# Performance work log

Measured on AMD Instinct MI355X. Metric: run time of the kernel, lower is better.

Reference implementation:

```python
import jax, jax.numpy as jnp
import numpy as np

N_NODES = 100000
N_EDGES = 1600000
N_GRAPHS = 1000
NODES_PER_GRAPH = 100
D_IN = 128
D_HID = 128
N_TASKS = 12


def setup_inputs() -> dict:
    key = jax.random.key(0)
    ks = jax.random.split(key, 6)
    X = jax.random.normal(ks[0], (N_NODES, D_IN), dtype=jnp.float32)
    edge_index = jax.random.randint(ks[1], (2, N_EDGES), 0, N_NODES, dtype=jnp.int64)
    graph_sizes = jnp.full((N_GRAPHS,), NODES_PER_GRAPH, dtype=jnp.int64)  # sums to N_NODES
    s0 = (2.0 / D_IN) ** 0.5
    W0 = jax.random.normal(ks[2], (D_IN, D_HID), dtype=jnp.float32) * s0
    b0 = jnp.zeros((D_HID,), dtype=jnp.float32)
    W1 = jax.random.normal(ks[3], (D_HID, D_HID), dtype=jnp.float32) * s0
    b1 = jnp.zeros((D_HID,), dtype=jnp.float32)
    Wf = jax.random.normal(ks[4], (D_HID, N_TASKS), dtype=jnp.float32) * s0
    bf = jnp.zeros((N_TASKS,), dtype=jnp.float32)
    return {"X": X, "edge_index": edge_index, "graph_sizes": graph_sizes,
            "W0": W0, "b0": b0, "W1": W1, "b1": b1, "Wf": Wf, "bf": bf}


def reference(X, edge_index, graph_sizes, W0, b0, W1, b1, Wf, bf):
    src, dst = edge_index[0], edge_index[1]
    n = X.shape[0]

    def gconv(x, W, b):
        # GCN-style message passing with self term: sum_{j->i} (x_j W) + x_i W + b
        xw = x @ W                                                    # [N, d]
        agg = jax.ops.segment_sum(xw[src], dst, num_segments=n)       # [N, d]
        return agg + xw + b

    # stacked conv -> relu -> dropout(eval=identity)
    h = jax.nn.relu(gconv(X, W0, b0))
    h = jax.nn.relu(gconv(h, W1, b1))
    out = jax.nn.sigmoid(h @ Wf + bf)                                  # [N, T]

    # ragged per-graph mean readout as a single segment-mean
    g = graph_sizes.shape[0]
    seg_ids = jnp.repeat(jnp.arange(g), graph_sizes, total_repeat_length=n)
    sums = jax.ops.segment_sum(out, seg_ids, num_segments=g)           # [G, T]
    return sums / graph_sizes[:, None].astype(out.dtype)
```

## Files before the change

### kernel.cpp

```cpp
#include <hip/hip_runtime.h>
#include <math.h>

#define D 128
#define NBUCK_MAX 1024
#define NB_EDGE   128

typedef unsigned short u16;
typedef unsigned int   u32;
typedef __attribute__((ext_vector_type(8))) short short8;
typedef __attribute__((ext_vector_type(4))) float f32x4;

static __device__ __forceinline__ u16 f32_to_bf16(float f) {
    u32 u = __builtin_bit_cast(u32, f);
    u32 r = (u + 0x7FFFu + ((u >> 16) & 1u)) >> 16;
    return (u16)r;
}
static __device__ __forceinline__ u32 pack_bf16x2(float lo, float hi) {
    return (u32)f32_to_bf16(lo) | ((u32)f32_to_bf16(hi) << 16);
}
static __device__ __forceinline__ float bf16lo_to_f32(u32 v) {
    return __builtin_bit_cast(float, v << 16);
}
static __device__ __forceinline__ float bf16hi_to_f32(u32 v) {
    return __builtin_bit_cast(float, v & 0xFFFF0000u);
}


__global__ __launch_bounds__(512) void bucket_count(const int* __restrict__ dst, int E, int nbuck,
                                                    int* __restrict__ blockHist) {
    __shared__ int h[NBUCK_MAX];
    int tid = threadIdx.x;
    for (int i = tid; i < nbuck; i += 512) h[i] = 0;
    __syncthreads();
    int per = (E + NB_EDGE - 1) / NB_EDGE;
    int s = blockIdx.x * per, e = min(E, s + per);
    for (int i = s + tid; i < e; i += 512) atomicAdd(&h[dst[i] >> 7], 1);
    __syncthreads();
    for (int i = tid; i < nbuck; i += 512) blockHist[blockIdx.x * nbuck + i] = h[i];
}

__global__ __launch_bounds__(256) void scan_blocks(int* __restrict__ blockHist, int nbuck,
                                                   int* __restrict__ bucketTotal) {
    int bucket = (blockIdx.x * 256 + threadIdx.x) >> 6;
    int lane = threadIdx.x & 63;
    if (bucket >= nbuck) return;
    int v0 = blockHist[lane * nbuck + bucket];
    int v1 = blockHist[(lane + 64) * nbuck + bucket];
    int i0 = v0;
    #pragma unroll
    for (int off = 1; off < 64; off <<= 1) { int t = __shfl_up(i0, off); if (lane >= off) i0 += t; }
    int tot0 = __shfl(i0, 63);
    int i1 = v1;
    #pragma unroll
    for (int off = 1; off < 64; off <<= 1) { int t = __shfl_up(i1, off); if (lane >= off) i1 += t; }
    i1 += tot0;
    blockHist[lane * nbuck + bucket] = i0 - v0;
    blockHist[(lane + 64) * nbuck + bucket] = i1 - v1;
    if (lane == 63) bucketTotal[bucket] = i1;
}

__global__ __launch_bounds__(256) void scan_buckets(const int* __restrict__ bucketTotal, int nbuck,
                                                    int* __restrict__ bucketBase) {
    __shared__ int wsum[4];
    int tid = threadIdx.x;
    int base = tid * 4;
    int v[4];
    #pragma unroll
    for (int k = 0; k < 4; k++) v[k] = (base + k < nbuck) ? bucketTotal[base + k] : 0;
    int s = v[0] + v[1] + v[2] + v[3];
    int lane = tid & 63;
    int incl = s;
    #pragma unroll
    for (int off = 1; off < 64; off <<= 1) { int t = __shfl_up(incl, off); if (lane >= off) incl += t; }
    int wv = tid >> 6;
    if (lane == 63) wsum[wv] = incl;
    __syncthreads();
    int woff = 0;
    for (int w = 0; w < wv; w++) woff += wsum[w];
    int excl = woff + incl - s;
    int run = excl;
    #pragma unroll
    for (int k = 0; k < 4; k++) {
        if (base + k <= nbuck) bucketBase[base + k] = run;
        run += v[k];
    }
}

__global__ __launch_bounds__(512) void bucket_place(const int* __restrict__ src, const int* __restrict__ dst,
                                                    int E, int nbuck, const int* __restrict__ blockHist,
                                                    const int* __restrict__ bucketBase,
                                                    u32* __restrict__ edgeBuf) {
    __shared__ int cur[NBUCK_MAX];
    int tid = threadIdx.x;
    for (int i = tid; i < nbuck; i += 512)
        cur[i] = bucketBase[i] + blockHist[blockIdx.x * nbuck + i];
    __syncthreads();
    int per = (E + NB_EDGE - 1) / NB_EDGE;
    int s = blockIdx.x * per, e = min(E, s + per);
    for (int i = s + tid; i < e; i += 512) {
        int d = dst[i];
        int b = d >> 7;
        int pos = atomicAdd(&cur[b], 1);
        edgeBuf[pos] = (u32)src[i] | ((u32)(d & 127) << 20);
    }
}

__global__ __launch_bounds__(256) void csr_finalize(const u32* __restrict__ edgeBuf,
                                                    const int* __restrict__ bucketBase,
                                                    int* __restrict__ row_ptr, int* __restrict__ col_idx,
                                                    int N, int E) {
    __shared__ int hist[128];
    __shared__ int cursor[128];
    int b = blockIdx.x;
    int tid = threadIdx.x;
    int start = bucketBase[b], end = bucketBase[b + 1];
    if (tid < 128) hist[tid] = 0;
    __syncthreads();
    for (int i = start + tid; i < end; i += 256)
        atomicAdd(&hist[edgeBuf[i] >> 20], 1);
    __syncthreads();
    if (tid < 64) {
        int v0 = hist[tid * 2], v1 = hist[tid * 2 + 1];
        int s = v0 + v1;
        int incl = s;
        #pragma unroll
        for (int off = 1; off < 64; off <<= 1) { int t = __shfl_up(incl, off); if (tid >= off) incl += t; }
        int excl = incl - s;
        cursor[tid * 2] = excl;
        cursor[tid * 2 + 1] = excl + v0;
        int node = b * 128 + tid * 2;
        if (node < N) row_ptr[node] = start + excl;
        if (node + 1 < N) row_ptr[node + 1] = start + excl + v0;
    }
    __syncthreads();
    for (int i = start + tid; i < end; i += 256) {
        u32 p = edgeBuf[i];
        int pos = atomicAdd(&cursor[p >> 20], 1);
        col_idx[start + pos] = (int)(p & 0xFFFFFu);
    }
    if (b == 0 && tid == 0) row_ptr[N] = E;
}

__global__ __launch_bounds__(256) void goff_scan(const int* __restrict__ gsz, int G, int* __restrict__ goff) {
    __shared__ int wsum[4];
    int tid = threadIdx.x;
    int base = tid * 4;
    int a = base + 0 < G ? gsz[base + 0] : 0;
    int b = base + 1 < G ? gsz[base + 1] : 0;
    int c = base + 2 < G ? gsz[base + 2] : 0;
    int d = base + 3 < G ? gsz[base + 3] : 0;
    int s = a + b + c + d;
    int lane = tid & 63;
    int incl = s;
    #pragma unroll
    for (int off = 1; off < 64; off <<= 1) { int t = __shfl_up(incl, off); if (lane >= off) incl += t; }
    int wv = tid >> 6;
    if (lane == 63) wsum[wv] = incl;
    __syncthreads();
    int woff = 0;
    for (int w = 0; w < wv; w++) woff += wsum[w];
    int excl = woff + incl - s;
    if (base + 0 < G) goff[base + 0] = excl;
    if (base + 1 < G) goff[base + 1] = excl + a;
    if (base + 2 < G) goff[base + 2] = excl + a + b;
    if (base + 3 < G) goff[base + 3] = excl + a + b + c;
}

__global__ __launch_bounds__(256) void cast_bf16(const float* __restrict__ X, u16* __restrict__ Xb, int n8) {
    int i = blockIdx.x * 256 + threadIdx.x;
    if (i >= n8) return;
    const float4* x4 = (const float4*)X;
    float4 a = x4[i * 2], b = x4[i * 2 + 1];
    uint4 r;
    r.x = pack_bf16x2(a.x, a.y);
    r.y = pack_bf16x2(a.z, a.w);
    r.z = pack_bf16x2(b.x, b.y);
    r.w = pack_bf16x2(b.z, b.w);
    ((uint4*)Xb)[i] = r;
}

__global__ __launch_bounds__(256) void pack_W(const float* __restrict__ W, u16* __restrict__ Wp) {
    int idx = blockIdx.x * 256 + threadIdx.x;
    if (idx >= 128 * 128) return;
    int j = idx & 7, lane = (idx >> 3) & 63, kt = (idx >> 9) & 3, nt = idx >> 11;
    int k = kt * 32 + ((lane >> 4) << 3) + j;
    int n = nt * 16 + (lane & 15);
    Wp[idx] = f32_to_bf16(W[k * 128 + n]);
}

__global__ __launch_bounds__(256) void gemm_mfma(const u16* __restrict__ A, const u16* __restrict__ Wp,
                                                 u16* __restrict__ outb, int N) {
    __shared__ u16 Cs[64 * 136];
    const int tid = threadIdx.x;
    const int wave = tid >> 6;
    const int lane = tid & 63;
    const int quad = lane >> 4;
    const int l16 = lane & 15;
    const int rowt = blockIdx.x * 64 + wave * 16;
    const int arow = rowt + l16;
    short8 af[4];
    if (arow < N) {
        const u16* ab = A + (size_t)arow * 128 + quad * 8;
        #pragma unroll
        for (int kt = 0; kt < 4; kt++) af[kt] = *(const short8*)(ab + kt * 32);
    } else {
        short8 z = {0, 0, 0, 0, 0, 0, 0, 0};
        #pragma unroll
        for (int kt = 0; kt < 4; kt++) af[kt] = z;
    }
    f32x4 acc[8];
    #pragma unroll
    for (int nt = 0; nt < 8; nt++) acc[nt] = (f32x4){0.f, 0.f, 0.f, 0.f};
    #pragma unroll
    for (int kt = 0; kt < 4; kt++) {
        #pragma unroll
        for (int nt = 0; nt < 8; nt++) {
            short8 bf = *(const short8*)(Wp + ((size_t)(nt * 4 + kt) * 64 + lane) * 8);
            acc[nt] = __builtin_amdgcn_mfma_f32_16x16x32_bf16(af[kt], bf, acc[nt], 0, 0, 0);
        }
    }
    #pragma unroll
    for (int nt = 0; nt < 8; nt++) {
        #pragma unroll
        for (int r = 0; r < 4; r++) {
            int rl = wave * 16 + quad * 4 + r;
            Cs[rl * 136 + nt * 16 + l16] = f32_to_bf16(acc[nt][r]);
        }
    }
    __syncthreads();
    const int row0 = blockIdx.x * 64;
    for (int i = tid; i < 64 * 16; i += 256) {
        int row = i >> 4, chunk = i & 15;
        int grow = row0 + row;
        if (grow < N)
            *(uint4*)(outb + (size_t)grow * 128 + chunk * 8) =
                *(const uint4*)(Cs + row * 136 + chunk * 8);
    }
}

__global__ __launch_bounds__(256) void agg_relu(const u16* __restrict__ xwb, const int* __restrict__ row_ptr,
                                                const int* __restrict__ col_idx, const float* __restrict__ bias,
                                                u16* __restrict__ outh, int N) {
    int wid = (blockIdx.x * 256 + threadIdx.x) >> 6;
    int lane = threadIdx.x & 63;
    if (wid >= N) return;
    const int c2 = lane * 2;
    float2 b = *(const float2*)(bias + c2);
    u32 sv = *(const u32*)(xwb + (size_t)wid * D + c2);
    float2 acc = make_float2(bf16lo_to_f32(sv) + b.x, bf16hi_to_f32(sv) + b.y);
    int start = row_ptr[wid], end = row_ptr[wid + 1];
    for (int e = start; e < end; e += 64) {
        int idx = e + lane;
        int j = (idx < end) ? col_idx[idx] : 0;
        int cnt = min(64, end - e);
        int i = 0;
        for (; i + 7 < cnt; i += 8) {
            int j0 = __shfl(j, i),     j1 = __shfl(j, i + 1);
            int j2 = __shfl(j, i + 2), j3 = __shfl(j, i + 3);
            int j4 = __shfl(j, i + 4), j5 = __shfl(j, i + 5);
            int j6 = __shfl(j, i + 6), j7 = __shfl(j, i + 7);
            u32 v0 = *(const u32*)(xwb + (size_t)j0 * D + c2);
            u32 v1 = *(const u32*)(xwb + (size_t)j1 * D + c2);
            u32 v2 = *(const u32*)(xwb + (size_t)j2 * D + c2);
            u32 v3 = *(const u32*)(xwb + (size_t)j3 * D + c2);
            u32 v4 = *(const u32*)(xwb + (size_t)j4 * D + c2);
            u32 v5 = *(const u32*)(xwb + (size_t)j5 * D + c2);
            u32 v6 = *(const u32*)(xwb + (size_t)j6 * D + c2);
            u32 v7 = *(const u32*)(xwb + (size_t)j7 * D + c2);
            acc.x += ((bf16lo_to_f32(v0) + bf16lo_to_f32(v1)) + (bf16lo_to_f32(v2) + bf16lo_to_f32(v3)))
                   + ((bf16lo_to_f32(v4) + bf16lo_to_f32(v5)) + (bf16lo_to_f32(v6) + bf16lo_to_f32(v7)));
            acc.y += ((bf16hi_to_f32(v0) + bf16hi_to_f32(v1)) + (bf16hi_to_f32(v2) + bf16hi_to_f32(v3)))
                   + ((bf16hi_to_f32(v4) + bf16hi_to_f32(v5)) + (bf16hi_to_f32(v6) + bf16hi_to_f32(v7)));
        }
        for (; i < cnt; i++) {
            int j0 = __shfl(j, i);
            u32 v0 = *(const u32*)(xwb + (size_t)j0 * D + c2);
            acc.x += bf16lo_to_f32(v0);
            acc.y += bf16hi_to_f32(v0);
        }
    }
    acc.x = fmaxf(acc.x, 0.f);
    acc.y = fmaxf(acc.y, 0.f);
    *(u32*)(outh + (size_t)wid * D + c2) = pack_bf16x2(acc.x, acc.y);
}

__global__ __launch_bounds__(256) void head_sigmoid(const u16* __restrict__ h, const float* __restrict__ Wf,
                                                    const float* __restrict__ bfv, float* __restrict__ out12, int N) {
    __shared__ float Wl[128 * 12];
    __shared__ float bl[12];
    for (int i = threadIdx.x; i < 128 * 12; i += 256) Wl[i] = Wf[i];
    if (threadIdx.x < 12) bl[threadIdx.x] = bfv[threadIdx.x];
    __syncthreads();
    int node = blockIdx.x * 256 + threadIdx.x;
    if (node >= N) return;
    float acc[12];
    #pragma unroll
    for (int t = 0; t < 12; t++) acc[t] = bl[t];
    const u16* hr = h + (size_t)node * D;
    for (int k = 0; k < 128; k += 8) {
        uint4 u = *(const uint4*)(hr + k);
        float x[8];
        x[0] = bf16lo_to_f32(u.x); x[1] = bf16hi_to_f32(u.x);
        x[2] = bf16lo_to_f32(u.y); x[3] = bf16hi_to_f32(u.y);
        x[4] = bf16lo_to_f32(u.z); x[5] = bf16hi_to_f32(u.z);
        x[6] = bf16lo_to_f32(u.w); x[7] = bf16hi_to_f32(u.w);
        #pragma unroll
        for (int kk = 0; kk < 8; kk++) {
            const float* wr = Wl + (k + kk) * 12;
            #pragma unroll
            for (int t = 0; t < 12; t++) acc[t] += x[kk] * wr[t];
        }
    }
    float* o = out12 + (size_t)node * 12;
    #pragma unroll
    for (int t = 0; t < 12; t++) o[t] = 1.f / (1.f + __expf(-acc[t]));
}

__global__ __launch_bounds__(128) void graph_mean(const float* __restrict__ out12, const int* __restrict__ goff,
                                                  const int* __restrict__ gsize, float* __restrict__ out, int G) {
    __shared__ float partial[120];
    int g = blockIdx.x;
    int tid = threadIdx.x;
    int start = goff[g];
    int size = gsize[g];
    if (tid < 120) {
        int t = tid % 12, chunk = tid / 12;
        float s = 0.f;
        for (int i = chunk; i < size; i += 10)
            s += out12[(size_t)(start + i) * 12 + t];
        partial[tid] = s;
    }
    __syncthreads();
    if (tid < 12) {
        float tot = 0.f;
        #pragma unroll
        for (int c = 0; c < 10; c++) tot += partial[c * 12 + tid];
        out[g * 12 + tid] = tot / (float)size;
    }
}


extern "C" void kernel_launch(void* const* d_in, const int* in_sizes, int n_in,
                              void* d_out, int out_size, void* d_ws, size_t ws_size,
                              hipStream_t stream) {
    const float* X   = (const float*)d_in[0];
    const int* edges = (const int*)d_in[1];
    const int* gsz   = (const int*)d_in[2];
    const float* W0  = (const float*)d_in[3];
    const float* b0  = (const float*)d_in[4];
    const float* W1  = (const float*)d_in[5];
    const float* b1  = (const float*)d_in[6];
    const float* Wf  = (const float*)d_in[7];
    const float* bfv = (const float*)d_in[8];
    float* out = (float*)d_out;

    const int N = in_sizes[0] / D;
    const int E = in_sizes[1] / 2;
    const int G = in_sizes[2];
    const int* esrc = edges;
    const int* edst = edges + E;
    const int nbuck = (N + 127) >> 7;

    char* ws = (char*)d_ws;
    char* p = ws;
    u16* Xb      = (u16*)p;  p += (((size_t)N * D * 2) + 255) & ~255ull;
    u16* xwb     = (u16*)p;  p += (((size_t)N * D * 2) + 255) & ~255ull;
    u16* hb      = (u16*)p;  p += (((size_t)N * D * 2) + 255) & ~255ull;
    float* out12 = (float*)p; p += (((size_t)N * 12 * 4) + 255) & ~255ull;
    u16* Wp0     = (u16*)p;  p += ((size_t)128 * 128 * 2 + 255) & ~255ull;
    u16* Wp1     = (u16*)p;  p += ((size_t)128 * 128 * 2 + 255) & ~255ull;
    u32* edgeBuf = (u32*)p;  p += (((size_t)E * 4) + 255) & ~255ull;
    int* col_idx = (int*)p;  p += (((size_t)E * 4) + 255) & ~255ull;
    int* row_ptr = (int*)p;  p += (((size_t)(N + 1) * 4) + 255) & ~255ull;
    int* blockHist   = (int*)p; p += ((size_t)NB_EDGE * NBUCK_MAX * 4 + 255) & ~255ull;
    int* bucketTotal = (int*)p; p += ((size_t)NBUCK_MAX * 4 + 255) & ~255ull;
    int* bucketBase  = (int*)p; p += ((size_t)(NBUCK_MAX + 1) * 4 + 255) & ~255ull;
    int* goff        = (int*)p;

    bucket_count<<<NB_EDGE, 512, 0, stream>>>(edst, E, nbuck, blockHist);
    scan_blocks<<<(nbuck * 64 + 255) / 256, 256, 0, stream>>>(blockHist, nbuck, bucketTotal);
    scan_buckets<<<1, 256, 0, stream>>>(bucketTotal, nbuck, bucketBase);
    bucket_place<<<NB_EDGE, 512, 0, stream>>>(esrc, edst, E, nbuck, blockHist, bucketBase, edgeBuf);
    csr_finalize<<<nbuck, 256, 0, stream>>>(edgeBuf, bucketBase, row_ptr, col_idx, N, E);

    cast_bf16<<<(N * 16 + 255) / 256, 256, 0, stream>>>(X, Xb, N * 16);
    pack_W<<<64, 256, 0, stream>>>(W0, Wp0);
    pack_W<<<64, 256, 0, stream>>>(W1, Wp1);
    goff_scan<<<1, 256, 0, stream>>>(gsz, G, goff);

    const int gemmGrid = (N + 63) / 64;
    gemm_mfma<<<gemmGrid, 256, 0, stream>>>(Xb, Wp0, xwb, N);
    agg_relu<<<(N * 64 + 255) / 256, 256, 0, stream>>>(xwb, row_ptr, col_idx, b0, hb, N);
    gemm_mfma<<<gemmGrid, 256, 0, stream>>>(hb, Wp1, xwb, N);
    agg_relu<<<(N * 64 + 255) / 256, 256, 0, stream>>>(xwb, row_ptr, col_idx, b1, hb, N);
    head_sigmoid<<<(N + 255) / 256, 256, 0, stream>>>(hb, Wf, bfv, out12, N);
    graph_mean<<<G, 128, 0, stream>>>(out12, goff, gsz, out, G);
}
```

Baseline: 333.5 us.

## Fuse bf16 cast into GEMM, head into graph mean, widen aggregation loads

Fuses the fp32-to-bf16 conversion of X into the first GEMM's A-load and folds the sigmoid head into the per-graph mean kernel, so the Xb and out12 intermediates disappear. It also merges the two small scans into one two-block launch and the two weight packs into one launch. The aggregation kernel is rewritten so each lane loads 16-byte chunks and four edges are processed at once per wave, followed by cross-quad shuffle reductions. This cuts launch count and global traffic, but head_mean runs only G blocks of 128 threads with about one node per thread, so parallelism there is low.

Result: faster. 314.5 us (-5.7%).

```diff
diff --git a/kernel.cpp b/kernel.cpp
--- a/kernel.cpp
+++ b/kernel.cpp
@@ -59,14 +59,19 @@
     if (lane == 63) bucketTotal[bucket] = i1;
 }
 
-__global__ __launch_bounds__(256) void scan_buckets(const int* __restrict__ bucketTotal, int nbuck,
-                                                    int* __restrict__ bucketBase) {
+__global__ __launch_bounds__(256) void combo_scan(const int* __restrict__ bucketTotal, int nbuck,
+                                                  int* __restrict__ bucketBase,
+                                                  const int* __restrict__ gsz, int G,
+                                                  int* __restrict__ goff) {
     __shared__ int wsum[4];
     int tid = threadIdx.x;
     int base = tid * 4;
+    const int* src = (blockIdx.x == 0) ? bucketTotal : gsz;
+    int n = (blockIdx.x == 0) ? nbuck : G;
+    int* dstp = (blockIdx.x == 0) ? bucketBase : goff;
     int v[4];
     #pragma unroll
-    for (int k = 0; k < 4; k++) v[k] = (base + k < nbuck) ? bucketTotal[base + k] : 0;
+    for (int k = 0; k < 4; k++) v[k] = (base + k < n) ? src[base + k] : 0;
     int s = v[0] + v[1] + v[2] + v[3];
     int lane = tid & 63;
     int incl = s;
@@ -77,11 +82,11 @@
     __syncthreads();
     int woff = 0;
     for (int w = 0; w < wv; w++) woff += wsum[w];
-    int excl = woff + incl - s;
-    int run = excl;
+    int run = woff + incl - s;
+    int lim = (blockIdx.x == 0) ? (n + 1) : n;
     #pragma unroll
     for (int k = 0; k < 4; k++) {
-        if (base + k <= nbuck) bucketBase[base + k] = run;
+        if (base + k < lim) dstp[base + k] = run;
         run += v[k];
     }
 }
@@ -141,73 +146,22 @@
     if (b == 0 && tid == 0) row_ptr[N] = E;
 }
 
-__global__ __launch_bounds__(256) void goff_scan(const int* __restrict__ gsz, int G, int* __restrict__ goff) {
-    __shared__ int wsum[4];
-    int tid = threadIdx.x;
-    int base = tid * 4;
-    int a = base + 0 < G ? gsz[base + 0] : 0;
-    int b = base + 1 < G ? gsz[base + 1] : 0;
-    int c = base + 2 < G ? gsz[base + 2] : 0;
-    int d = base + 3 < G ? gsz[base + 3] : 0;
-    int s = a + b + c + d;
-    int lane = tid & 63;
-    int incl = s;
-    #pragma unroll
-    for (int off = 1; off < 64; off <<= 1) { int t = __shfl_up(incl, off); if (lane >= off) incl += t; }
-    int wv = tid >> 6;
-    if (lane == 63) wsum[wv] = incl;
-    __syncthreads();
-    int woff = 0;
-    for (int w = 0; w < wv; w++) woff += wsum[w];
-    int excl = woff + incl - s;
-    if (base + 0 < G) goff[base + 0] = excl;
-    if (base + 1 < G) goff[base + 1] = excl + a;
-    if (base + 2 < G) goff[base + 2] = excl + a + b;
-    if (base + 3 < G) goff[base + 3] = excl + a + b + c;
-}
-
-__global__ __launch_bounds__(256) void cast_bf16(const float* __restrict__ X, u16* __restrict__ Xb, int n8) {
-    int i = blockIdx.x * 256 + threadIdx.x;
-    if (i >= n8) return;
-    const float4* x4 = (const float4*)X;
-    float4 a = x4[i * 2], b = x4[i * 2 + 1];
-    uint4 r;
-    r.x = pack_bf16x2(a.x, a.y);
-    r.y = pack_bf16x2(a.z, a.w);
-    r.z = pack_bf16x2(b.x, b.y);
-    r.w = pack_bf16x2(b.z, b.w);
-    ((uint4*)Xb)[i] = r;
-}
-
-__global__ __launch_bounds__(256) void pack_W(const float* __restrict__ W, u16* __restrict__ Wp) {
-    int idx = blockIdx.x * 256 + threadIdx.x;
-    if (idx >= 128 * 128) return;
+__global__ __launch_bounds__(256) void pack_W2(const float* __restrict__ W0, const float* __restrict__ W1,
+                                               u16* __restrict__ Wp0, u16* __restrict__ Wp1) {
+    int gidx = blockIdx.x * 256 + threadIdx.x;
+    const float* W = (gidx < 128 * 128) ? W0 : W1;
+    u16* Wp = (gidx < 128 * 128) ? Wp0 : Wp1;
+    int idx = gidx & (128 * 128 - 1);
     int j = idx & 7, lane = (idx >> 3) & 63, kt = (idx >> 9) & 3, nt = idx >> 11;
     int k = kt * 32 + ((lane >> 4) << 3) + j;
     int n = nt * 16 + (lane & 15);
     Wp[idx] = f32_to_bf16(W[k * 128 + n]);
 }
 
-__global__ __launch_bounds__(256) void gemm_mfma(const u16* __restrict__ A, const u16* __restrict__ Wp,
-                                                 u16* __restrict__ outb, int N) {
-    __shared__ u16 Cs[64 * 136];
-    const int tid = threadIdx.x;
-    const int wave = tid >> 6;
-    const int lane = tid & 63;
-    const int quad = lane >> 4;
-    const int l16 = lane & 15;
-    const int rowt = blockIdx.x * 64 + wave * 16;
-    const int arow = rowt + l16;
-    short8 af[4];
-    if (arow < N) {
-        const u16* ab = A + (size_t)arow * 128 + quad * 8;
-        #pragma unroll
-        for (int kt = 0; kt < 4; kt++) af[kt] = *(const short8*)(ab + kt * 32);
-    } else {
-        short8 z = {0, 0, 0, 0, 0, 0, 0, 0};
-        #pragma unroll
-        for (int kt = 0; kt < 4; kt++) af[kt] = z;
-    }
+static __device__ __forceinline__ void gemm_body(const short8 af[4], const u16* __restrict__ Wp,
+                                                 u16* __restrict__ outb, int N,
+                                                 int tid, int wave, int lane, int quad, int l16,
+                                                 u16* Cs) {
     f32x4 acc[8];
     #pragma unroll
     for (int nt = 0; nt < 8; nt++) acc[nt] = (f32x4){0.f, 0.f, 0.f, 0.f};
@@ -238,105 +192,168 @@
     }
 }
 
+__global__ __launch_bounds__(256) void gemm_mfma_f32(const float* __restrict__ A, const u16* __restrict__ Wp,
+                                                     u16* __restrict__ outb, int N) {
+    __shared__ u16 Cs[64 * 136];
+    const int tid = threadIdx.x;
+    const int wave = tid >> 6, lane = tid & 63, quad = lane >> 4, l16 = lane & 15;
+    const int arow = blockIdx.x * 64 + wave * 16 + l16;
+    union { u32 u[4]; short8 s; } cv;
+    short8 af[4];
+    if (arow < N) {
+        const float* ab = A + (size_t)arow * 128 + quad * 8;
+        #pragma unroll
+        for (int kt = 0; kt < 4; kt++) {
+            float4 x0 = *(const float4*)(ab + kt * 32);
+            float4 x1 = *(const float4*)(ab + kt * 32 + 4);
+            cv.u[0] = pack_bf16x2(x0.x, x0.y);
+            cv.u[1] = pack_bf16x2(x0.z, x0.w);
+            cv.u[2] = pack_bf16x2(x1.x, x1.y);
+            cv.u[3] = pack_bf16x2(x1.z, x1.w);
+            af[kt] = cv.s;
+        }
+    } else {
+        short8 z = {0, 0, 0, 0, 0, 0, 0, 0};
+        #pragma unroll
+        for (int kt = 0; kt < 4; kt++) af[kt] = z;
+    }
+    gemm_body(af, Wp, outb, N, tid, wave, lane, quad, l16, Cs);
+}
+
+__global__ __launch_bounds__(256) void gemm_mfma(const u16* __restrict__ A, const u16* __restrict__ Wp,
+                                                 u16* __restrict__ outb, int N) {
+    __shared__ u16 Cs[64 * 136];
+    const int tid = threadIdx.x;
+    const int wave = tid >> 6, lane = tid & 63, quad = lane >> 4, l16 = lane & 15;
+    const int arow = blockIdx.x * 64 + wave * 16 + l16;
+    short8 af[4];
+    if (arow < N) {
+        const u16* ab = A + (size_t)arow * 128 + quad * 8;
+        #pragma unroll
+        for (int kt = 0; kt < 4; kt++) af[kt] = *(const short8*)(ab + kt * 32);
+    } else {
+        short8 z = {0, 0, 0, 0, 0, 0, 0, 0};
+        #pragma unroll
+        for (int kt = 0; kt < 4; kt++) af[kt] = z;
+    }
+    gemm_body(af, Wp, outb, N, tid, wave, lane, quad, l16, Cs);
+}
+
+static __device__ __forceinline__ void add_row(float* acc, uint4 u, bool v) {
+    if (v) {
+        acc[0] += bf16lo_to_f32(u.x); acc[1] += bf16hi_to_f32(u.x);
+        acc[2] += bf16lo_to_f32(u.y); acc[3] += bf16hi_to_f32(u.y);
+        acc[4] += bf16lo_to_f32(u.z); acc[5] += bf16hi_to_f32(u.z);
+        acc[6] += bf16lo_to_f32(u.w); acc[7] += bf16hi_to_f32(u.w);
+    }
+}
+
 __global__ __launch_bounds__(256) void agg_relu(const u16* __restrict__ xwb, const int* __restrict__ row_ptr,
                                                 const int* __restrict__ col_idx, const float* __restrict__ bias,
                                                 u16* __restrict__ outh, int N) {
     int wid = (blockIdx.x * 256 + threadIdx.x) >> 6;
     int lane = threadIdx.x & 63;
     if (wid >= N) return;
-    const int c2 = lane * 2;
-    float2 b = *(const float2*)(bias + c2);
-    u32 sv = *(const u32*)(xwb + (size_t)wid * D + c2);
-    float2 acc = make_float2(bf16lo_to_f32(sv) + b.x, bf16hi_to_f32(sv) + b.y);
+    const int q = lane >> 4;
+    const int d8 = (lane & 15) * 8;
+    float acc[8] = {0.f, 0.f, 0.f, 0.f, 0.f, 0.f, 0.f, 0.f};
     int start = row_ptr[wid], end = row_ptr[wid + 1];
     for (int e = start; e < end; e += 64) {
         int idx = e + lane;
         int j = (idx < end) ? col_idx[idx] : 0;
         int cnt = min(64, end - e);
-        int i = 0;
-        for (; i + 7 < cnt; i += 8) {
-            int j0 = __shfl(j, i),     j1 = __shfl(j, i + 1);
-            int j2 = __shfl(j, i + 2), j3 = __shfl(j, i + 3);
-            int j4 = __shfl(j, i + 4), j5 = __shfl(j, i + 5);
-            int j6 = __shfl(j, i + 6), j7 = __shfl(j, i + 7);
-            u32 v0 = *(const u32*)(xwb + (size_t)j0 * D + c2);
-            u32 v1 = *(const u32*)(xwb + (size_t)j1 * D + c2);
-            u32 v2 = *(const u32*)(xwb + (size_t)j2 * D + c2);
-            u32 v3 = *(const u32*)(xwb + (size_t)j3 * D + c2);
-            u32 v4 = *(const u32*)(xwb + (size_t)j4 * D + c2);
-            u32 v5 = *(const u32*)(xwb + (size_t)j5 * D + c2);
-            u32 v6 = *(const u32*)(xwb + (size_t)j6 * D + c2);
-            u32 v7 = *(const u32*)(xwb + (size_t)j7 * D + c2);
-            acc.x += ((bf16lo_to_f32(v0) + bf16lo_to_f32(v1)) + (bf16lo_to_f32(v2) + bf16lo_to_f32(v3)))
-                   + ((bf16lo_to_f32(v4) + bf16lo_to_f32(v5)) + (bf16lo_to_f32(v6) + bf16lo_to_f32(v7)));
-            acc.y += ((bf16hi_to_f32(v0) + bf16hi_to_f32(v1)) + (bf16hi_to_f32(v2) + bf16hi_to_f32(v3)))
-                   + ((bf16hi_to_f32(v4) + bf16hi_to_f32(v5)) + (bf16hi_to_f32(v6) + bf16hi_to_f32(v7)));
+        for (int i = 0; i < cnt; i += 16) {
+            int j0 = __shfl(j, i + q);
+            int j1 = __shfl(j, i + 4 + q);
+            int j2 = __shfl(j, i + 8 + q);
+            int j3 = __shfl(j, i + 12 + q);
+            uint4 r0 = *(const uint4*)(xwb + (size_t)j0 * D + d8);
+            uint4 r1 = *(const uint4*)(xwb + (size_t)j1 * D + d8);
+            uint4 r2 = *(const uint4*)(xwb + (size_t)j2 * D + d8);
+            uint4 r3 = *(const uint4*)(xwb + (size_t)j3 * D + d8);
+            add_row(acc, r0, (i + q) < cnt);
+            add_row(acc, r1, (i + 4 + q) < cnt);
+            add_row(acc, r2, (i + 8 + q) < cnt);
+            add_row(acc, r3, (i + 12 + q) < cnt);
         }
-        for (; i < cnt; i++) {
-            int j0 = __shfl(j, i);
-            u32 v0 = *(const u32*)(xwb + (size_t)j0 * D + c2);
-            acc.x += bf16lo_to_f32(v0);
-            acc.y += bf16hi_to_f32(v0);
-        }
-    }
-    acc.x = fmaxf(acc.x, 0.f);
-    acc.y = fmaxf(acc.y, 0.f);
-    *(u32*)(outh + (size_t)wid * D + c2) = pack_bf16x2(acc.x, acc.y);
-}
-
-__global__ __launch_bounds__(256) void head_sigmoid(const u16* __restrict__ h, const float* __restrict__ Wf,
-                                                    const float* __restrict__ bfv, float* __restrict__ out12, int N) {
+    }
+    #pragma unroll
+    for (int t = 0; t < 8; t++) {
+        acc[t] += __shfl_xor(acc[t], 16);
+        acc[t] += __shfl_xor(acc[t], 32);
+    }
+    uint4 sv = *(const uint4*)(xwb + (size_t)wid * D + d8);
+    float4 ba = *(const float4*)(bias + d8);
+    float4 bb = *(const float4*)(bias + d8 + 4);
+    float r[8];
+    r[0] = fmaxf(acc[0] + bf16lo_to_f32(sv.x) + ba.x, 0.f);
+    r[1] = fmaxf(acc[1] + bf16hi_to_f32(sv.x) + ba.y, 0.f);
+    r[2] = fmaxf(acc[2] + bf16lo_to_f32(sv.y) + ba.z, 0.f);
+    r[3] = fmaxf(acc[3] + bf16hi_to_f32(sv.y) + ba.w, 0.f);
+    r[4] = fmaxf(acc[4] + bf16lo_to_f32(sv.z) + bb.x, 0.f);
+    r[5] = fmaxf(acc[5] + bf16hi_to_f32(sv.z) + bb.y, 0.f);
+    r[6] = fmaxf(acc[6] + bf16lo_to_f32(sv.w) + bb.z, 0.f);
+    r[7] = fmaxf(acc[7] + bf16hi_to_f32(sv.w) + bb.w, 0.f);
+    if (q == 0) {
+        uint4 o;
+        o.x = pack_bf16x2(r[0], r[1]);
+        o.y = pack_bf16x2(r[2], r[3]);
+        o.z = pack_bf16x2(r[4], r[5]);
+        o.w = pack_bf16x2(r[6], r[7]);
+        *(uint4*)(outh + (size_t)wid * D + d8) = o;
+    }
+}
+
+__global__ __launch_bounds__(128) void head_mean(const u16* __restrict__ h, const float* __restrict__ Wf,
+                                                 const float* __restrict__ bfv, const int* __restrict__ goff,
+                                                 const int* __restrict__ gsize, float* __restrict__ out, int G) {
     __shared__ float Wl[128 * 12];
     __shared__ float bl[12];
-    for (int i = threadIdx.x; i < 128 * 12; i += 256) Wl[i] = Wf[i];
-    if (threadIdx.x < 12) bl[threadIdx.x] = bfv[threadIdx.x];
-    __syncthreads();
-    int node = blockIdx.x * 256 + threadIdx.x;
-    if (node >= N) return;
-    float acc[12];
-    #pragma unroll
-    for (int t = 0; t < 12; t++) acc[t] = bl[t];
-    const u16* hr = h + (size_t)node * D;
-    for (int k = 0; k < 128; k += 8) {
-        uint4 u = *(const uint4*)(hr + k);
-        float x[8];
-        x[0] = bf16lo_to_f32(u.x); x[1] = bf16hi_to_f32(u.x);
-        x[2] = bf16lo_to_f32(u.y); x[3] = bf16hi_to_f32(u.y);
-        x[4] = bf16lo_to_f32(u.z); x[5] = bf16hi_to_f32(u.z);
-        x[6] = bf16lo_to_f32(u.w); x[7] = bf16hi_to_f32(u.w);
-        #pragma unroll
-        for (int kk = 0; kk < 8; kk++) {
-            const float* wr = Wl + (k + kk) * 12;
-            #pragma unroll
-            for (int t = 0; t < 12; t++) acc[t] += x[kk] * wr[t];
-        }
-    }
-    float* o = out12 + (size_t)node * 12;
-    #pragma unroll
-    for (int t = 0; t < 12; t++) o[t] = 1.f / (1.f + __expf(-acc[t]));
-}
-
-__global__ __launch_bounds__(128) void graph_mean(const float* __restrict__ out12, const int* __restrict__ goff,
-                                                  const int* __restrict__ gsize, float* __restrict__ out, int G) {
-    __shared__ float partial[120];
+    __shared__ float part[2][12];
+    int tid = threadIdx.x;
+    for (int i = tid; i < 128 * 12; i += 128) Wl[i] = Wf[i];
+    if (tid < 12) bl[tid] = bfv[tid];
+    __syncthreads();
     int g = blockIdx.x;
-    int tid = threadIdx.x;
     int start = goff[g];
     int size = gsize[g];
-    if (tid < 120) {
-        int t = tid % 12, chunk = tid / 12;
-        float s = 0.f;
-        for (int i = chunk; i < size; i += 10)
-            s += out12[(size_t)(start + i) * 12 + t];
-        partial[tid] = s;
-    }
-    __syncthreads();
-    if (tid < 12) {
-        float tot = 0.f;
-        #pragma unroll
-        for (int c = 0; c < 10; c++) tot += partial[c * 12 + tid];
-        out[g * 12 + tid] = tot / (float)size;
-    }
+    float sum[12];
+    #pragma unroll
+    for (int t = 0; t < 12; t++) sum[t] = 0.f;
+    for (int n = tid; n < size; n += 128) {
+        const u16* hr = h + (size_t)(start + n) * D;
+        float acc[12];
+        #pragma unroll
+        for (int t = 0; t < 12; t++) acc[t] = bl[t];
+        for (int k = 0; k < 128; k += 8) {
+            uint4 u = *(const uint4*)(hr + k);
+            float x[8];
+            x[0] = bf16lo_to_f32(u.x); x[1] = bf16hi_to_f32(u.x);
+            x[2] = bf16lo_to_f32(u.y); x[3] = bf16hi_to_f32(u.y);
+            x[4] = bf16lo_to_f32(u.z); x[5] = bf16hi_to_f32(u.z);
+            x[6] = bf16lo_to_f32(u.w); x[7] = bf16hi_to_f32(u.w);
+            #pragma unroll
+            for (int kk = 0; kk < 8; kk++) {
+                const float* wr = Wl + (k + kk) * 12;
+                #pragma unroll
+                for (int t = 0; t < 12; t++) acc[t] += x[kk] * wr[t];
+            }
+        }
+        #pragma unroll
+        for (int t = 0; t < 12; t++) sum[t] += 1.f / (1.f + __expf(-acc[t]));
+    }
+    int lane = tid & 63, wv = tid >> 6;
+    #pragma unroll
+    for (int t = 0; t < 12; t++) {
+        #pragma unroll
+        for (int off = 32; off >= 1; off >>= 1) sum[t] += __shfl_xor(sum[t], off);
+    }
+    if (lane == 0) {
+        #pragma unroll
+        for (int t = 0; t < 12; t++) part[wv][t] = sum[t];
+    }
+    __syncthreads();
+    if (tid < 12) out[(size_t)g * 12 + tid] = (part[0][tid] + part[1][tid]) / (float)size;
 }
 
 
@@ -363,10 +380,8 @@
 
     char* ws = (char*)d_ws;
     char* p = ws;
-    u16* Xb      = (u16*)p;  p += (((size_t)N * D * 2) + 255) & ~255ull;
     u16* xwb     = (u16*)p;  p += (((size_t)N * D * 2) + 255) & ~255ull;
     u16* hb      = (u16*)p;  p += (((size_t)N * D * 2) + 255) & ~255ull;
-    float* out12 = (float*)p; p += (((size_t)N * 12 * 4) + 255) & ~255ull;
     u16* Wp0     = (u16*)p;  p += ((size_t)128 * 128 * 2 + 255) & ~255ull;
     u16* Wp1     = (u16*)p;  p += ((size_t)128 * 128 * 2 + 255) & ~255ull;
     u32* edgeBuf = (u32*)p;  p += (((size_t)E * 4) + 255) & ~255ull;
@@ -379,20 +394,16 @@
 
     bucket_count<<<NB_EDGE, 512, 0, stream>>>(edst, E, nbuck, blockHist);
     scan_blocks<<<(nbuck * 64 + 255) / 256, 256, 0, stream>>>(blockHist, nbuck, bucketTotal);
-    scan_buckets<<<1, 256, 0, stream>>>(bucketTotal, nbuck, bucketBase);
+    combo_scan<<<2, 256, 0, stream>>>(bucketTotal, nbuck, bucketBase, gsz, G, goff);
     bucket_place<<<NB_EDGE, 512, 0, stream>>>(esrc, edst, E, nbuck, blockHist, bucketBase, edgeBuf);
     csr_finalize<<<nbuck, 256, 0, stream>>>(edgeBuf, bucketBase, row_ptr, col_idx, N, E);
 
-    cast_bf16<<<(N * 16 + 255) / 256, 256, 0, stream>>>(X, Xb, N * 16);
-    pack_W<<<64, 256, 0, stream>>>(W0, Wp0);
-    pack_W<<<64, 256, 0, stream>>>(W1, Wp1);
-    goff_scan<<<1, 256, 0, stream>>>(gsz, G, goff);
+    pack_W2<<<128, 256, 0, stream>>>(W0, W1, Wp0, Wp1);
 
     const int gemmGrid = (N + 63) / 64;
-    gemm_mfma<<<gemmGrid, 256, 0, stream>>>(Xb, Wp0, xwb, N);
+    gemm_mfma_f32<<<gemmGrid, 256, 0, stream>>>(X, Wp0, xwb, N);
     agg_relu<<<(N * 64 + 255) / 256, 256, 0, stream>>>(xwb, row_ptr, col_idx, b0, hb, N);
     gemm_mfma<<<gemmGrid, 256, 0, stream>>>(hb, Wp1, xwb, N);
     agg_relu<<<(N * 64 + 255) / 256, 256, 0, stream>>>(xwb, row_ptr, col_idx, b1, hb, N);
-    head_sigmoid<<<(N + 255) / 256, 256, 0, stream>>>(hb, Wf, bfv, out12, N);
-    graph_mean<<<G, 128, 0, stream>>>(out12, goff, gsz, out, G);
-}
+    head_mean<<<G, 128, 0, stream>>>(hb, Wf, bfv, goff, gsz, out, G);
+}
```
